# Kernel tuning notes

Measured on AMD Instinct MI355X. Metric: run time of the kernel, lower is better.

## Reference

```python
import jax, jax.numpy as jnp
import numpy as np

B, N = 256, 20000

def setup_inputs() -> dict:
    key = jax.random.key(0)
    k1, k2 = jax.random.split(key)
    x_in = jax.random.normal(k1, (B, 1, N, 4), dtype=jnp.float32)
    weights = jax.random.uniform(k2, (B, N), dtype=jnp.float32)
    return {"x_in": x_in, "weights": weights}

def reference(x_in, weights):
    # weighted_8points: x_in [B,1,N,4] -> e_hat [B,9]
    b, _, n, _ = x_in.shape
    xx = x_in[:, 0, :, :]                      # [B,N,4] = (x1, y1, x2, y2)
    x1, y1, x2, y2 = xx[..., 0], xx[..., 1], xx[..., 2], xx[..., 3]
    ones = jnp.ones_like(x1)
    # Epipolar design matrix rows: [x2*x1, x2*y1, x2, y2*x1, y2*y1, y2, x1, y1, 1]
    X = jnp.stack([x2 * x1, x2 * y1, x2,
                   y2 * x1, y2 * y1, y2,
                   x1, y1, ones], axis=-1)      # [B,N,9]
    wX = weights[:, :, None] * X                # [B,N,9]
    XwX = jnp.einsum('bni,bnj->bij', X, wX)     # [B,9,9] symmetric
    # batch_symeig: eigenvectors ascending by eigenvalue; smallest -> column 0
    _, v = jnp.linalg.eigh(XwX)                 # [B,9,9]
    e_hat = v[:, :, 0]                          # [B,9]
    e_hat = e_hat / jnp.linalg.norm(e_hat, axis=1, keepdims=True)
    return e_hat
```

## Files before the change

kernel.cpp:

```cpp
#include <hip/hip_runtime.h>
#include <math.h>

#define BATCH 256
#define NPTS  20000


__device__ __forceinline__ float f_sign(float a, float b) {
    return (b >= 0.0f) ? fabsf(a) : -fabsf(a);
}

__device__ __forceinline__ float slapy2(float xx, float yy) {
    float xa = fabsf(xx), ya = fabsf(yy);
    float w_ = fmaxf(xa, ya), z_ = fminf(xa, ya);
    if (z_ == 0.0f) return w_;
    float t = z_ / w_;
    return w_ * sqrtf(1.0f + t * t);
}

__device__ __forceinline__ float rdl(float v, int i) {
    return __int_as_float(__builtin_amdgcn_readlane(__float_as_int(v), i));
}

__device__ __forceinline__ void slartg(float f, float g, float* cs, float* sn, float* r) {
    if (g == 0.0f) { *cs = 1.0f; *sn = 0.0f; *r = f; }
    else if (f == 0.0f) { *cs = 0.0f; *sn = (g >= 0.0f) ? 1.0f : -1.0f; *r = fabsf(g); }
    else {
        float dd2 = sqrtf(f * f + g * g);
        *cs = fabsf(f) / dd2;
        *r  = f_sign(dd2, f);
        *sn = g / (*r);
    }
}

__device__ void slaev2(float a, float b, float c_, float* rt1, float* rt2,
                       float* cs1, float* sn1) {
    float sm = a + c_;
    float df = a - c_;
    float adf = fabsf(df);
    float tb = b + b;
    float ab = fabsf(tb);
    float acmx, acmn;
    if (fabsf(a) > fabsf(c_)) { acmx = a; acmn = c_; } else { acmx = c_; acmn = a; }
    float rt;
    if (adf > ab)      { float t = ab / adf; rt = adf * sqrtf(1.0f + t * t); }
    else if (adf < ab) { float t = adf / ab; rt = ab * sqrtf(1.0f + t * t); }
    else               { rt = ab * sqrtf(2.0f); }
    int sgn1;
    if (sm < 0.0f) {
        *rt1 = 0.5f * (sm - rt); sgn1 = -1;
        *rt2 = (acmx / (*rt1)) * acmn - (b / (*rt1)) * b;
    } else if (sm > 0.0f) {
        *rt1 = 0.5f * (sm + rt); sgn1 = 1;
        *rt2 = (acmx / (*rt1)) * acmn - (b / (*rt1)) * b;
    } else {
        *rt1 = 0.5f * rt; *rt2 = -0.5f * rt; sgn1 = 1;
    }
    float cs; int sgn2;
    if (df >= 0.0f) { cs = df + rt; sgn2 = 1; } else { cs = df - rt; sgn2 = -1; }
    float acs = fabsf(cs);
    if (acs > ab) {
        float ct = -tb / cs;
        *sn1 = 1.0f / sqrtf(1.0f + ct * ct);
        *cs1 = ct * (*sn1);
    } else {
        if (ab == 0.0f) { *cs1 = 1.0f; *sn1 = 0.0f; }
        else {
            float tn = -cs / tb;
            *cs1 = 1.0f / sqrtf(1.0f + tn * tn);
            *sn1 = tn * (*cs1);
        }
    }
    if (sgn1 == sgn2) { float tn = *cs1; *cs1 = -(*sn1); *sn1 = tn; }
}

#define APPLY_QL() do { \
    _Pragma("unroll") \
    for (int jz = 8; jz >= 1; --jz) { \
        float cj = rdl(r_cw, jz), sj = rdl(r_sw, jz); \
        float tmpz = zz[jz + 1]; \
        zz[jz + 1] = cj * tmpz - sj * zz[jz]; \
        zz[jz]     = sj * tmpz + cj * zz[jz]; \
    } } while (0)

#define APPLY_QR() do { \
    _Pragma("unroll") \
    for (int jz = 1; jz <= 8; ++jz) { \
        float cj = rdl(r_cw, jz), sj = rdl(r_sw, jz); \
        float tmpz = zz[jz + 1]; \
        zz[jz + 1] = cj * tmpz - sj * zz[jz]; \
        zz[jz]     = sj * tmpz + cj * zz[jz]; \
    } } while (0)

__global__ __launch_bounds__(512) void fused_kernel(
    const float4* __restrict__ x, const float* __restrict__ wgt,
    float* __restrict__ out)
{
    const int n = 9;
    int b = blockIdx.x;
    int tid = threadIdx.x;
    int lane = tid & 63;
    int rw = tid >> 6;

    __shared__ float red[16][45];
    __shared__ float A[10][10];
    __shared__ float Zl[10][10];
    __shared__ float ddl[11], eel[11], tau[10], wvl[10], zvl[10];

    for (int half = 0; half < 2; ++half) {
        int v = rw * 2 + half;
        int chunk = v >> 2, wvc = v & 3;
        float acc[45];
#pragma unroll
        for (int k = 0; k < 45; ++k) acc[k] = 0.0f;

        const float4* xb = x + (size_t)b * NPTS;
        const float*  wb = wgt + (size_t)b * NPTS;
        int base = chunk * 5000;
        for (int nn = base + wvc * 64 + lane; nn < base + 5000; nn += 256) {
            float4 vv = xb[nn];
            float wt = wb[nn];
            float X[9];
            X[0] = vv.z * vv.x; X[1] = vv.z * vv.y; X[2] = vv.z;
            X[3] = vv.w * vv.x; X[4] = vv.w * vv.y; X[5] = vv.w;
            X[6] = vv.x;        X[7] = vv.y;        X[8] = 1.0f;
            int idx = 0;
#pragma unroll
            for (int j = 0; j < 9; ++j) {
                float wXj = wt * X[j];
#pragma unroll
                for (int i = j; i < 9; ++i) {
                    acc[idx] += X[i] * wXj;
                    ++idx;
                }
            }
        }
#pragma unroll
        for (int k = 0; k < 45; ++k) {
            float vred = acc[k];
            for (int off = 32; off > 0; off >>= 1)
                vred += __shfl_down(vred, off, 64);
            acc[k] = vred;
        }
        if (lane == 0) {
#pragma unroll
            for (int k = 0; k < 45; ++k) red[v][k] = acc[k];
        }
    }
    __syncthreads();
    if (tid >= 64) return;

    if (lane < 45) {
        double p0 = (double)red[0][lane]  + (double)red[1][lane]
                  + (double)red[2][lane]  + (double)red[3][lane];
        double p1 = (double)red[4][lane]  + (double)red[5][lane]
                  + (double)red[6][lane]  + (double)red[7][lane];
        double p2 = (double)red[8][lane]  + (double)red[9][lane]
                  + (double)red[10][lane] + (double)red[11][lane];
        double p3 = (double)red[12][lane] + (double)red[13][lane]
                  + (double)red[14][lane] + (double)red[15][lane];
        double s = ((p0 + p1) + p2) + p3;
        int idx = lane, j = 1;
        while (idx >= 10 - j) { idx -= (10 - j); ++j; }
        int i = j + idx;
        A[i][j] = (float)s;
    }

    for (int i = 1; i <= n - 1; ++i) {
        float alpha = A[i + 1][i];
        float ssq = 0.0f;
        for (int k = i + 2; k <= n; ++k) ssq += A[k][i] * A[k][i];
        float xnorm = sqrtf(ssq);
        float taui;
        if (xnorm == 0.0f) {
            taui = 0.0f;
            if (lane == 0) eel[i] = alpha;
        } else {
            float beta = -f_sign(slapy2(alpha, xnorm), alpha);
            taui = (beta - alpha) / beta;
            float sc = 1.0f / (alpha - beta);
            if (lane < 8 - i) {
                int k = i + 2 + lane;
                A[k][i] *= sc;
            }
            if (lane == 0) eel[i] = beta;
        }
        if (taui != 0.0f) {
            if (lane < 9 - i) {
                int r2 = i + 1 + lane;
                float s2 = 0.0f;
                for (int c2 = i + 1; c2 <= n; ++c2) {
                    float aval = (r2 >= c2) ? A[r2][c2] : A[c2][r2];
                    float vc = (c2 == i + 1) ? 1.0f : A[c2][i];
                    s2 += aval * vc;
                }
                wvl[r2] = taui * s2;
            }
            float dot = 0.0f;
            for (int k = i + 1; k <= n; ++k) {
                float vk = (k == i + 1) ? 1.0f : A[k][i];
                dot += wvl[k] * vk;
            }
            float alpha2 = -0.5f * taui * dot;
            if (lane < 9 - i) {
                int k = i + 1 + lane;
                float vk = (k == i + 1) ? 1.0f : A[k][i];
                wvl[k] += alpha2 * vk;
            }
            int kk = 9 - i;
            int cnt = kk * (kk + 1) / 2;
            if (lane < cnt) {
                int idx = lane, cc = 0;
                while (idx >= kk - cc) { idx -= (kk - cc); ++cc; }
                int c2 = i + 1 + cc;
                int r2 = c2 + idx;
                float vr = (r2 == i + 1) ? 1.0f : A[r2][i];
                float vc = (c2 == i + 1) ? 1.0f : A[c2][i];
                A[r2][c2] -= vr * wvl[c2] + wvl[r2] * vc;
            }
        }
        if (lane == 0) { ddl[i] = A[i][i]; tau[i] = taui; }
    }
    if (lane == 0) ddl[n] = A[n][n];

    float r_dd, r_ee, r_cw, r_sw;
    float zz[10];
    r_dd = 0.0f; r_ee = 0.0f;
    if (lane >= 1 && lane <= 9) r_dd = ddl[lane];
    if (lane >= 1 && lane <= 8) r_ee = eel[lane];
#pragma unroll
    for (int c0 = 1; c0 <= 9; ++c0) zz[c0] = (lane == c0) ? 1.0f : 0.0f;

    const float eps    = 5.9604645e-8f;
    const float eps2   = eps * eps;
    const float safmin = 1.17549435e-38f;
    const float safmax = 1.0f / 1.17549435e-38f;
    const float ssfmax = sqrtf(safmax) / 3.0f;
    const float ssfmin = sqrtf(safmin) / eps2;

    int nmaxit = n * 30, jtot = 0;
    int l1 = 1, nm1 = n - 1;
    int l, m, lsv, lend, lendsv, iscale;
    float anorm, p, g, r, c, s, f, btmp, rt1, rt2, tst, mul;

L10:
    if (l1 > n) goto L160;
    if (l1 > 1) r_ee = (lane == l1 - 1) ? 0.0f : r_ee;
    if (l1 <= nm1) {
        for (m = l1; m <= nm1; ++m) {
            tst = fabsf(rdl(r_ee, m));
            if (tst == 0.0f) goto L30;
            if (tst <= (sqrtf(fabsf(rdl(r_dd, m))) * sqrtf(fabsf(rdl(r_dd, m + 1)))) * eps) {
                r_ee = (lane == m) ? 0.0f : r_ee;
                goto L30;
            }
        }
    }
    m = n;
L30:
    l = l1; lsv = l; lend = m; lendsv = lend; l1 = m + 1;
    if (lend == l) goto L10;

    anorm = 0.0f;
    for (int k = l; k <= lend; ++k) anorm = fmaxf(anorm, fabsf(rdl(r_dd, k)));
    for (int k = l; k <= lend - 1; ++k) anorm = fmaxf(anorm, fabsf(rdl(r_ee, k)));
    iscale = 0;
    if (anorm == 0.0f) goto L10;
    if (anorm > ssfmax) {
        iscale = 1; mul = ssfmax / anorm;
        r_dd = (lane >= l && lane <= lend)     ? r_dd * mul : r_dd;
        r_ee = (lane >= l && lane <= lend - 1) ? r_ee * mul : r_ee;
    } else if (anorm < ssfmin) {
        iscale = 2; mul = ssfmin / anorm;
        r_dd = (lane >= l && lane <= lend)     ? r_dd * mul : r_dd;
        r_ee = (lane >= l && lane <= lend - 1) ? r_ee * mul : r_ee;
    }

    if (fabsf(rdl(r_dd, lend)) < fabsf(rdl(r_dd, l))) { lend = lsv; l = lendsv; }

    if (lend > l) {
L40:
        if (l != lend) {
            for (m = l; m <= lend - 1; ++m) {
                tst = fabsf(rdl(r_ee, m)); tst = tst * tst;
                if (tst <= (eps2 * fabsf(rdl(r_dd, m))) * fabsf(rdl(r_dd, m + 1)) + safmin) goto L60;
            }
        }
        m = lend;
L60:
        if (m < lend) r_ee = (lane == m) ? 0.0f : r_ee;
        p = rdl(r_dd, l);
        if (m == l) goto L80;
        if (m == l + 1) {
            slaev2(rdl(r_dd, l), rdl(r_ee, l), rdl(r_dd, l + 1), &rt1, &rt2, &c, &s);
            r_cw = 1.0f; r_sw = 0.0f;
            r_cw = (lane == l) ? c : r_cw;
            r_sw = (lane == l) ? s : r_sw;
            APPLY_QL();
            r_dd = (lane == l) ? rt1 : ((lane == l + 1) ? rt2 : r_dd);
            r_ee = (lane == l) ? 0.0f : r_ee;
            l += 2;
            if (l <= lend) goto L40;
            goto L140;
        }
        if (jtot == nmaxit) goto L140;
        ++jtot;
        g = (rdl(r_dd, l + 1) - p) / (2.0f * rdl(r_ee, l));
        r = slapy2(g, 1.0f);
        g = rdl(r_dd, m) - p + rdl(r_ee, l) / (g + f_sign(r, g));
        s = 1.0f; c = 1.0f; p = 0.0f;
        r_cw = 1.0f; r_sw = 0.0f;
        for (int i = m - 1; i >= l; --i) {
            float ei = rdl(r_ee, i);
            f = s * ei; btmp = c * ei;
            slartg(g, f, &c, &s, &r);
            if (i != m - 1) r_ee = (lane == i + 1) ? r : r_ee;
            g = rdl(r_dd, i + 1) - p;
            r = (rdl(r_dd, i) - g) * s + 2.0f * c * btmp;
            p = s * r;
            r_dd = (lane == i + 1) ? (g + p) : r_dd;
            g = c * r - btmp;
            r_cw = (lane == i) ? c : r_cw;
            r_sw = (lane == i) ? (-s) : r_sw;
        }
        APPLY_QL();
        r_dd = (lane == l) ? (r_dd - p) : r_dd;
        r_ee = (lane == l) ? g : r_ee;
        goto L40;
L80:
        r_dd = (lane == l) ? p : r_dd;
        l = l + 1;
        if (l <= lend) goto L40;
        goto L140;
    } else {
L90:
        if (l != lend) {
            for (m = l; m >= lend + 1; --m) {
                tst = fabsf(rdl(r_ee, m - 1)); tst = tst * tst;
                if (tst <= (eps2 * fabsf(rdl(r_dd, m))) * fabsf(rdl(r_dd, m - 1)) + safmin) goto L110;
            }
        }
        m = lend;
L110:
        if (m > lend) r_ee = (lane == m - 1) ? 0.0f : r_ee;
        p = rdl(r_dd, l);
        if (m == l) goto L130;
        if (m == l - 1) {
            slaev2(rdl(r_dd, l - 1), rdl(r_ee, l - 1), rdl(r_dd, l), &rt1, &rt2, &c, &s);
            r_cw = 1.0f; r_sw = 0.0f;
            r_cw = (lane == l - 1) ? c : r_cw;
            r_sw = (lane == l - 1) ? s : r_sw;
            APPLY_QR();
            r_dd = (lane == l - 1) ? rt1 : ((lane == l) ? rt2 : r_dd);
            r_ee = (lane == l - 1) ? 0.0f : r_ee;
            l -= 2;
            if (l >= lend) goto L90;
            goto L140;
        }
        if (jtot == nmaxit) goto L140;
        ++jtot;
        g = (rdl(r_dd, l - 1) - p) / (2.0f * rdl(r_ee, l - 1));
        r = slapy2(g, 1.0f);
        g = rdl(r_dd, m) - p + rdl(r_ee, l - 1) / (g + f_sign(r, g));
        s = 1.0f; c = 1.0f; p = 0.0f;
        r_cw = 1.0f; r_sw = 0.0f;
        for (int i = m; i <= l - 1; ++i) {
            float ei = rdl(r_ee, i);
            f = s * ei; btmp = c * ei;
            slartg(g, f, &c, &s, &r);
            if (i != m) r_ee = (lane == i - 1) ? r : r_ee;
            g = rdl(r_dd, i) - p;
            r = (rdl(r_dd, i + 1) - g) * s + 2.0f * c * btmp;
            p = s * r;
            r_dd = (lane == i) ? (g + p) : r_dd;
            g = c * r - btmp;
            r_cw = (lane == i) ? c : r_cw;
            r_sw = (lane == i) ? s : r_sw;
        }
        APPLY_QR();
        r_dd = (lane == l) ? (r_dd - p) : r_dd;
        r_ee = (lane == l - 1) ? g : r_ee;
        goto L90;
L130:
        r_dd = (lane == l) ? p : r_dd;
        l = l - 1;
        if (l >= lend) goto L90;
        goto L140;
    }

L140:
    if (iscale == 1) {
        mul = anorm / ssfmax;
        r_dd = (lane >= lsv && lane <= lendsv)     ? r_dd * mul : r_dd;
        r_ee = (lane >= lsv && lane <= lendsv - 1) ? r_ee * mul : r_ee;
    } else if (iscale == 2) {
        mul = anorm / ssfmin;
        r_dd = (lane >= lsv && lane <= lendsv)     ? r_dd * mul : r_dd;
        r_ee = (lane >= lsv && lane <= lendsv - 1) ? r_ee * mul : r_ee;
    }
    if (jtot < nmaxit) goto L10;
    goto L160;

L160:
    if (lane >= 1 && lane <= 9) {
#pragma unroll
        for (int c0 = 1; c0 <= 9; ++c0) Zl[lane][c0] = zz[c0];
    }

    for (int ii = 2; ii <= n; ++ii) {
        int i = ii - 1, k = i;
        p = rdl(r_dd, i);
        for (int j = ii; j <= n; ++j) {
            float dj = rdl(r_dd, j);
            if (dj < p) { k = j; p = dj; }
        }
        if (k != i) {
            float di = rdl(r_dd, i);
            r_dd = (lane == k) ? di : r_dd;
            r_dd = (lane == i) ? p  : r_dd;
            if (lane >= 1 && lane <= 9) {
                float t = Zl[lane][i]; Zl[lane][i] = Zl[lane][k]; Zl[lane][k] = t;
            }
        }
    }

    if (lane < 9) zvl[lane + 1] = Zl[lane + 1][1];
    for (int i2 = n - 1; i2 >= 1; --i2) {
        float ti = tau[i2];
        if (ti != 0.0f) {
            float dotp = zvl[i2 + 1];
            for (int k = i2 + 2; k <= n; ++k) dotp += A[k][i2] * zvl[k];
            float t = ti * dotp;
            if (lane < 9 - i2) {
                int k = i2 + 1 + lane;
                float upd = (k == i2 + 1) ? t : t * A[k][i2];
                zvl[k] -= upd;
            }
        }
    }
    {
        float nrm = 0.0f;
        for (int row = 1; row <= n; ++row) nrm += zvl[row] * zvl[row];
        nrm = sqrtf(nrm);
        if (lane < 9) out[(size_t)b * 9 + lane] = zvl[lane + 1] / nrm;
    }
}

extern "C" void kernel_launch(void* const* d_in, const int* in_sizes, int n_in,
                              void* d_out, int out_size, void* d_ws, size_t ws_size,
                              hipStream_t stream) {
    const float4* x = (const float4*)d_in[0];
    const float*  w = (const float*)d_in[1];
    float* out = (float*)d_out;
    (void)d_ws; (void)ws_size;

    fused_kernel<<<dim3(BATCH), dim3(512), 0, stream>>>(x, w, out);
}
```

Measured before the change: 193.5 us.

## Use 1024-thread blocks and wave-parallel ballot scans in tridiagonal QL

```diff
diff --git a/kernel.cpp b/kernel.cpp
--- a/kernel.cpp
+++ b/kernel.cpp
@@ -19,6 +19,15 @@
 
 __device__ __forceinline__ float rdl(float v, int i) {
     return __int_as_float(__builtin_amdgcn_readlane(__float_as_int(v), i));
+}
+
+__device__ __forceinline__ float rfl(float v) {
+    return __int_as_float(__builtin_amdgcn_readfirstlane(__float_as_int(v)));
+}
+
+__device__ __forceinline__ unsigned long long lanerange(int lo, int hi) {
+    if (hi < lo) return 0ull;
+    return (1ull << (hi + 1)) - (1ull << lo);
 }
 
 __device__ __forceinline__ void slartg(float f, float g, float* cs, float* sn, float* r) {
@@ -91,7 +100,7 @@
         zz[jz]     = sj * tmpz + cj * zz[jz]; \
     } } while (0)
 
-__global__ __launch_bounds__(512) void fused_kernel(
+__global__ __launch_bounds__(1024) void fused_kernel(
     const float4* __restrict__ x, const float* __restrict__ wgt,
     float* __restrict__ out)
 {
@@ -106,9 +115,8 @@
     __shared__ float Zl[10][10];
     __shared__ float ddl[11], eel[11], tau[10], wvl[10], zvl[10];
 
-    for (int half = 0; half < 2; ++half) {
-        int v = rw * 2 + half;
-        int chunk = v >> 2, wvc = v & 3;
+    {
+        int chunk = rw >> 2, wvc = rw & 3;
         float acc[45];
 #pragma unroll
         for (int k = 0; k < 45; ++k) acc[k] = 0.0f;
@@ -143,7 +151,7 @@
         }
         if (lane == 0) {
 #pragma unroll
-            for (int k = 0; k < 45; ++k) red[v][k] = acc[k];
+            for (int k = 0; k < 45; ++k) red[rw][k] = acc[k];
         }
     }
     __syncthreads();
@@ -240,29 +248,32 @@
     int nmaxit = n * 30, jtot = 0;
     int l1 = 1, nm1 = n - 1;
     int l, m, lsv, lend, lendsv, iscale;
-    float anorm, p, g, r, c, s, f, btmp, rt1, rt2, tst, mul;
+    float anorm, p, g, r, c, s, f, btmp, rt1, rt2, mul;
 
 L10:
     if (l1 > n) goto L160;
     if (l1 > 1) r_ee = (lane == l1 - 1) ? 0.0f : r_ee;
     if (l1 <= nm1) {
-        for (m = l1; m <= nm1; ++m) {
-            tst = fabsf(rdl(r_ee, m));
-            if (tst == 0.0f) goto L30;
-            if (tst <= (sqrtf(fabsf(rdl(r_dd, m))) * sqrtf(fabsf(rdl(r_dd, m + 1)))) * eps) {
-                r_ee = (lane == m) ? 0.0f : r_ee;
-                goto L30;
-            }
-        }
-    }
-    m = n;
-L30:
+        float dmp1 = __shfl_down(r_dd, 1, 64);
+        bool pred = (fabsf(r_ee) <= (sqrtf(fabsf(r_dd)) * sqrtf(fabsf(dmp1))) * eps);
+        unsigned long long msk = __ballot(pred) & lanerange(l1, nm1);
+        if (msk) {
+            m = (int)__builtin_ctzll(msk);
+            r_ee = (lane == m) ? 0.0f : r_ee;
+        } else m = n;
+    } else m = n;
+
     l = l1; lsv = l; lend = m; lendsv = lend; l1 = m + 1;
     if (lend == l) goto L10;
 
-    anorm = 0.0f;
-    for (int k = l; k <= lend; ++k) anorm = fmaxf(anorm, fabsf(rdl(r_dd, k)));
-    for (int k = l; k <= lend - 1; ++k) anorm = fmaxf(anorm, fabsf(rdl(r_ee, k)));
+    {
+        float av = 0.0f;
+        if (lane >= l && lane <= lend)     av = fabsf(r_dd);
+        if (lane >= l && lane <= lend - 1) av = fmaxf(av, fabsf(r_ee));
+        for (int off = 32; off > 0; off >>= 1)
+            av = fmaxf(av, __shfl_down(av, off, 64));
+        anorm = rfl(av);
+    }
     iscale = 0;
     if (anorm == 0.0f) goto L10;
     if (anorm > ssfmax) {
@@ -279,15 +290,16 @@
 
     if (lend > l) {
 L40:
-        if (l != lend) {
-            for (m = l; m <= lend - 1; ++m) {
-                tst = fabsf(rdl(r_ee, m)); tst = tst * tst;
-                if (tst <= (eps2 * fabsf(rdl(r_dd, m))) * fabsf(rdl(r_dd, m + 1)) + safmin) goto L60;
-            }
-        }
-        m = lend;
-L60:
-        if (m < lend) r_ee = (lane == m) ? 0.0f : r_ee;
+        {
+            float dmp1 = __shfl_down(r_dd, 1, 64);
+            float t2 = fabsf(r_ee); t2 = t2 * t2;
+            bool pred = (t2 <= (eps2 * fabsf(r_dd)) * fabsf(dmp1) + safmin);
+            unsigned long long msk = __ballot(pred) & lanerange(l, lend - 1);
+            if (msk) {
+                m = (int)__builtin_ctzll(msk);
+                r_ee = (lane == m) ? 0.0f : r_ee;
+            } else m = lend;
+        }
         p = rdl(r_dd, l);
         if (m == l) goto L80;
         if (m == l + 1) {
@@ -333,15 +345,17 @@
         goto L140;
     } else {
 L90:
-        if (l != lend) {
-            for (m = l; m >= lend + 1; --m) {
-                tst = fabsf(rdl(r_ee, m - 1)); tst = tst * tst;
-                if (tst <= (eps2 * fabsf(rdl(r_dd, m))) * fabsf(rdl(r_dd, m - 1)) + safmin) goto L110;
-            }
-        }
-        m = lend;
-L110:
-        if (m > lend) r_ee = (lane == m - 1) ? 0.0f : r_ee;
+        {
+            float djp1 = __shfl_down(r_dd, 1, 64);
+            float t2 = fabsf(r_ee); t2 = t2 * t2;
+            bool pred = (t2 <= (eps2 * fabsf(djp1)) * fabsf(r_dd) + safmin);
+            unsigned long long msk = __ballot(pred) & lanerange(lend, l - 1);
+            if (msk) {
+                int j = 63 - (int)__builtin_clzll(msk);
+                m = j + 1;
+                r_ee = (lane == j) ? 0.0f : r_ee;
+            } else m = lend;
+        }
         p = rdl(r_dd, l);
         if (m == l) goto L130;
         if (m == l - 1) {
@@ -453,5 +467,5 @@
     float* out = (float*)d_out;
     (void)d_ws; (void)ws_size;
 
-    fused_kernel<<<dim3(BATCH), dim3(512), 0, stream>>>(x, w, out);
-}
+    fused_kernel<<<dim3(BATCH), dim3(1024), 0, stream>>>(x, w, out);
+}
```

New measurement: 182.4 us. 5.7% less time.
